# Performance work log

Hardware: AMD Instinct MI355X
Metric: run time of the kernel (lower is better)

## Reference

```python
import jax, jax.numpy as jnp
import numpy as np

S = 30000      # num sessions (= num clicks)
ND = 300000    # num displayed rows (10 per session)
F = 64         # f_dim
I = 500        # item_size (news_cnt_short)
PW = 10        # pw_dim
BAND = 20      # pw_band_size
H = 256        # mlp hidden


def setup_inputs() -> dict:
    key = jax.random.key(0)
    ks = jax.random.split(key, 8)
    per = ND // S  # disp rows per session
    disp_sec = jnp.repeat(jnp.arange(S, dtype=jnp.int64), per)          # sorted, every segment nonempty
    click_sub = jnp.arange(S, dtype=jnp.int64) * per                     # one clicked disp row per session
    # banded lower-triangular cumulative-sum indices: row r attends to cols r-0..r-(BAND-1) (clipped at 0)
    rows = jnp.repeat(jnp.arange(S, dtype=jnp.int64), BAND)
    offs = jnp.tile(jnp.arange(BAND, dtype=jnp.int64), S)
    cols = jnp.clip(rows - offs, 0)
    tril_idx = jnp.stack([rows, cols], axis=1)                            # [NT,2]
    click_items = jax.random.randint(ks[0], (S,), 0, I, dtype=jnp.int64)
    disp_items = jax.random.randint(ks[1], (ND,), 0, I, dtype=jnp.int64)
    return {
        'disp_current_feature': jax.random.normal(ks[2], (ND, F), dtype=jnp.float32),
        'Xs_clicked': jax.random.normal(ks[3], (S, F), dtype=jnp.float32),
        'W1': jax.random.normal(ks[4], (F * PW + F, H), dtype=jnp.float32) * 0.05,
        'b1': jnp.zeros((H,), jnp.float32),
        'W2': jax.random.normal(ks[5], (H, H), dtype=jnp.float32) * 0.05,
        'b2': jnp.zeros((H,), jnp.float32),
        'W3': jax.random.normal(ks[6], (H, 1), dtype=jnp.float32) * 0.05,
        'b3': jnp.zeros((1,), jnp.float32),
        'cumsum_tril_indices': tril_idx,
        'cumsum_tril_value_indices': offs,
        'disp_2d_split_sec_ind': disp_sec,
        'click_2d_subindex': click_sub,
        'click_indices': jnp.stack([jnp.arange(S, dtype=jnp.int64), click_items], axis=1),
        'disp_indices': jnp.stack([disp_sec, disp_items], axis=1),
        'section_length': S,
        'item_size': I,
        'pw_dim': PW,
        'band_size': BAND,
    }


def reference(disp_current_feature, Xs_clicked, W1, b1, W2, b2, W3, b3,
              cumsum_tril_indices, cumsum_tril_value_indices,
              disp_2d_split_sec_ind, click_2d_subindex,
              click_indices, disp_indices,
              section_length, item_size, pw_dim, band_size):
    # position weights (fixed 1e-4 as in original forward), gathered per sparse entry
    position_weight = jnp.full((band_size,), 1e-4, dtype=jnp.float32)
    vals = position_weight[cumsum_tril_value_indices]                     # [NT]
    # sparse [S,S] matmul with Xs_clicked expressed as gather + segment_sum (same math as dense matmul)
    contrib = vals[:, None] * Xs_clicked[cumsum_tril_indices[:, 1]]       # [NT,F]
    hist = jax.ops.segment_sum(contrib, cumsum_tril_indices[:, 0], num_segments=section_length)  # [S,F]
    # the pw_dim copies are identical (same position_weight each loop iteration)
    concat_history = jnp.concatenate([hist] * pw_dim, axis=1)             # [S, PW*F]
    disp_hist = concat_history[disp_2d_split_sec_ind]                     # [ND, PW*F]
    feats = jnp.concatenate([disp_hist, disp_current_feature], axis=1)    # [ND, (PW+1)*F]
    h = jax.nn.elu(feats @ W1 + b1)
    h = jax.nn.elu(h @ W2 + b2)
    u_disp = h @ W3 + b3                                                  # [ND,1]
    exp_u = jnp.exp(u_disp)
    sum_exp = jax.ops.segment_sum(exp_u, disp_2d_split_sec_ind, num_segments=section_length)  # [S,1]
    sum_click_u = u_disp[click_2d_subindex]                               # [S,1]
    loss_sum = jnp.sum(-sum_click_u + jnp.log(sum_exp + 1.0))
    click_tensor = jnp.zeros((section_length, item_size), jnp.float32).at[
        click_indices[:, 0], click_indices[:, 1]].add(1.0)
    event_cnt = jnp.sum(click_tensor)
    loss = loss_sum / event_cnt
    dense_exp = jnp.zeros((section_length, item_size), jnp.float32).at[
        disp_indices[:, 0], disp_indices[:, 1]].add(exp_u[:, 0])
    argmax_click = jnp.argmax(click_tensor, axis=1)
    argmax_disp = jnp.argmax(dense_exp, axis=1)
    top2 = jax.lax.top_k(dense_exp, 2)[1]                                 # [S,2]
    p1_sum = jnp.sum(argmax_click == argmax_disp)
    p2_sum = jnp.sum(argmax_click[:, None] == top2)
    precision_1 = p1_sum / event_cnt
    precision_2 = p2_sum / event_cnt
    return (loss, precision_1, precision_2, loss_sum, p1_sum, p2_sum, event_cnt)
```

## Files before the change

### kernel.cpp

```cpp
#include <hip/hip_runtime.h>
#include <hip/hip_bf16.h>

#define TPB 256

typedef _Float16 f16;
typedef f16 f16x8 __attribute__((ext_vector_type(8)));
typedef f16 f16x4 __attribute__((ext_vector_type(4)));
typedef f16 f16x2 __attribute__((ext_vector_type(2)));
typedef float f32x16 __attribute__((ext_vector_type(16)));
typedef unsigned int uint;

union F16x8U { f16x8 v; uint4 q; };
union F16x4U { f16x4 v; uint2 q; };

__device__ __forceinline__ float elu_f(float z) {
    return z > 0.f ? z : __expf(z) - 1.f;
}

__global__ void prepw0_kernel(const float* __restrict__ W1, int PW,
                              f16* __restrict__ W1sT_hi,
                              float* __restrict__ lossTot, int* __restrict__ cnts) {
    int t = blockIdx.x * blockDim.x + threadIdx.x;
    if (t < 16384) {
        int k = t >> 8, n = t & 255;
        float s = 0.f;
        for (int p = 0; p < PW; ++p) s += W1[(size_t)(p * 64 + k) * 256 + n];
        W1sT_hi[n * 64 + k] = (f16)s;
    } else if (t == 16384) {
        lossTot[0] = 0.f;
        cnts[0] = 0; cnts[1] = 0; cnts[2] = 0;
    }
}

__global__ __launch_bounds__(TPB, 4) void hist_ahist_kernel(
    const float* __restrict__ Xs, const int* __restrict__ tril,
    const f16* __restrict__ W1sT_hi, const float* __restrict__ b1,
    f16* __restrict__ Ah16, int S, int band,
    const float* __restrict__ W1, const float* __restrict__ W2, int PW,
    f16* __restrict__ W1bT_hi, f16* __restrict__ W2sw,
    int HB)
{
    __shared__ f16 hB[128 * 72];

    const int tid = threadIdx.x;

    if ((int)blockIdx.x >= HB) {
        int t = (blockIdx.x - HB) * TPB + tid;
        if (t < 16384) {
            int k = t >> 8, n = t & 255;
            W1bT_hi[n * 64 + k] = (f16)W1[(size_t)(PW * 64 + k) * 256 + n];
        } else {
            int t2 = t - 16384;
            int k = t2 >> 8, n = t2 & 255;
            W2sw[(size_t)(k >> 3) * 2048 + n * 8 + (k & 7)] = (f16)W2[(size_t)k * 256 + n];
        }
        return;
    }

    const int SB = blockIdx.x * 128;

    {
        const int f = tid & 63, w = tid >> 6;
        const int rl0 = w * 32;
        const int rg0 = SB + rl0;
        float sum = 0.f;
        #pragma unroll
        for (int o = 0; o < 20; ++o) {
            int gi = rg0 - o; if (gi < 0) gi = 0;
            sum += Xs[(size_t)gi * 64 + f];
        }
        hB[rl0 * 72 + f] = (f16)(sum * 1e-4f);
        for (int rl = rl0 + 1; rl < rl0 + 32; ++rl) {
            int rg = SB + rl;
            int rgc = rg <= S - 1 ? rg : S - 1;
            int gs = rg - 20; if (gs < 0) gs = 0; if (gs > S - 1) gs = S - 1;
            sum += Xs[(size_t)rgc * 64 + f] - Xs[(size_t)gs * 64 + f];
            hB[rl * 72 + f] = (f16)(sum * 1e-4f);
        }
    }
    __syncthreads();

    const int w = tid >> 6;
    const int l = tid & 63, lr = l & 31, hh = l >> 5;
    const int nt0 = 2 * w;

    #pragma unroll
    for (int st = 0; st < 4; ++st) {
        int sgl = st * 32 + lr;
        F16x8U Bh[4];
        #pragma unroll
        for (int ks = 0; ks < 4; ++ks)
            Bh[ks].q = *(const uint4*)&hB[sgl * 72 + ks * 16 + 8 * hh];
        int sg = SB + sgl;
        #pragma unroll
        for (int jn = 0; jn < 2; ++jn) {
            int nt = nt0 + jn;
            f32x16 acc;
            #pragma unroll
            for (int rq = 0; rq < 4; ++rq) {
                float4 bq = *(const float4*)&b1[nt * 32 + rq * 8 + 4 * hh];
                acc[rq * 4 + 0] = bq.x; acc[rq * 4 + 1] = bq.y;
                acc[rq * 4 + 2] = bq.z; acc[rq * 4 + 3] = bq.w;
            }
            const f16* ah = W1sT_hi + (size_t)(nt * 32 + lr) * 64 + 8 * hh;
            #pragma unroll
            for (int ks = 0; ks < 4; ++ks) {
                f16x8 Ah = *(const f16x8*)(ah + ks * 16);
                acc = __builtin_amdgcn_mfma_f32_32x32x16_f16(Ah, Bh[ks].v, acc, 0, 0, 0);
            }
            if (sg < S) {
                F16x8U o0, o1;
                #pragma unroll
                for (int i = 0; i < 8; ++i) {
                    o0.v[i] = (f16)acc[i];
                    o1.v[i] = (f16)acc[8 + i];
                }
                f16* op = Ah16 + (((size_t)sg * 8 + nt) * 2 + hh) * 16;
                *(uint4*)op = o0.q;
                *(uint4*)(op + 8) = o1.q;
            }
        }
    }
}

__global__ __launch_bounds__(512, 4) void mlp18_kernel(
    const float* __restrict__ dispF, const f16* __restrict__ Ah16,
    const f16* __restrict__ W1bT_hi,
    const f16* __restrict__ W2sw,
    const float* __restrict__ b2, const float* __restrict__ W3,
    const float* __restrict__ b3, float* __restrict__ u,
    int ND, int per, float inv_per)
{
    __shared__ uint4 frag[4][16][64];
    f16* dstage = (f16*)&frag[3][0][0];

    const int tid = threadIdx.x;
    const int w = tid >> 6, l = tid & 63, lr = l & 31, hh = l >> 5;
    const int RB = blockIdx.x * 128;
    const int nt = w;

    #pragma unroll
    for (int r = 0; r < 4; ++r) {
        int i = r * 512 + tid;
        int row = i >> 4, q = i & 15;
        int k8 = q >> 1;
        int rg = RB + row; if (rg > ND - 1) rg = ND - 1;
        float4 v = *(const float4*)&dispF[(size_t)rg * 64 + q * 4];
        F16x4U o;
        o.v[0] = (f16)v.x; o.v[1] = (f16)v.y; o.v[2] = (f16)v.z; o.v[3] = (f16)v.w;
        *(uint2*)&dstage[(size_t)(((row >> 5) * 8 + k8) * 256)
                         + ((row & 31) ^ k8) * 8 + (q & 1) * 4] = o.q;
    }

    const f16* a1h = W1bT_hi + (size_t)(nt * 32 + lr) * 64 + 8 * hh;
    f16x8 A1h[4];
    #pragma unroll
    for (int ks = 0; ks < 4; ++ks) A1h[ks] = *(const f16x8*)(a1h + ks * 16);

    const f16* w2p = W2sw + (size_t)hh * 2048 + (size_t)(nt * 32 + lr) * 8;
    f16x8 W2p[4];
    #pragma unroll
    for (int kp = 0; kp < 4; ++kp) W2p[kp] = *(const f16x8*)(w2p + (size_t)kp * 4096);

    int srow[4];
    #pragma unroll
    for (int st = 0; st < 4; ++st) {
        int rg = RB + st * 32 + lr;
        int rgc = rg <= ND - 1 ? rg : ND - 1;
        int sr = (int)((float)rgc * inv_per);
        sr += ((sr + 1) * per <= rgc) ? 1 : 0;
        srow[st] = sr;
    }

    __syncthreads();

    f16x8 Db[2][4];
    uint4 AhP[2][2];
    #pragma unroll
    for (int b = 0; b < 2; ++b) {
        #pragma unroll
        for (int ks = 0; ks < 4; ++ks) {
            int k8 = ks * 2 + hh;
            Db[b][ks] = *(const f16x8*)&dstage[(size_t)((b * 8 + k8) * 256) + (lr ^ k8) * 8];
        }
        const f16* ap = Ah16 + (((size_t)srow[b] * 8 + nt) * 2 + hh) * 16;
        AhP[b][0] = *(const uint4*)ap;
        AhP[b][1] = *(const uint4*)(ap + 8);
    }

    #pragma unroll
    for (int st = 0; st < 4; ++st) {
        f32x16 acc;
        {
            F16x8U u0, u1; u0.q = AhP[st & 1][0]; u1.q = AhP[st & 1][1];
            #pragma unroll
            for (int i = 0; i < 8; ++i) {
                acc[i] = (float)u0.v[i];
                acc[8 + i] = (float)u1.v[i];
            }
        }
        if (st + 2 < 4) {
            const f16* ap = Ah16 + (((size_t)srow[st + 2] * 8 + nt) * 2 + hh) * 16;
            AhP[st & 1][0] = *(const uint4*)ap;
            AhP[st & 1][1] = *(const uint4*)(ap + 8);
        }
        #pragma unroll
        for (int ks = 0; ks < 4; ++ks) {
            acc = __builtin_amdgcn_mfma_f32_32x32x16_f16(A1h[ks], Db[st & 1][ks], acc, 0, 0, 0);
        }
        if (st + 2 < 4) {
            #pragma unroll
            for (int ks = 0; ks < 4; ++ks) {
                int k8 = ks * 2 + hh;
                Db[st & 1][ks] = *(const f16x8*)&dstage[
                    (size_t)(((st + 2) * 8 + k8) * 256) + (lr ^ k8) * 8];
            }
        }

        uint p[4][2];
        #pragma unroll
        for (int rq = 0; rq < 4; ++rq) {
            #pragma unroll
            for (int jj = 0; jj < 2; ++jj) {
                float a = elu_f(acc[rq * 4 + 2 * jj]);
                float b = elu_f(acc[rq * 4 + 2 * jj + 1]);
                f16x2 hp; hp[0] = (f16)a; hp[1] = (f16)b;
                p[rq][jj] = __builtin_bit_cast(uint, hp);
            }
        }
        #pragma unroll
        for (int c = 0; c < 2; ++c) {
            uint s0 = hh ? p[2 * c][0] : p[2 * c + 1][0];
            uint s1 = hh ? p[2 * c][1] : p[2 * c + 1][1];
            uint r0 = __shfl_xor(s0, 32, 64);
            uint r1 = __shfl_xor(s1, 32, 64);
            uint4 B;
            B.x = hh ? r0 : p[2 * c][0];
            B.y = hh ? r1 : p[2 * c][1];
            B.z = hh ? p[2 * c + 1][0] : r0;
            B.w = hh ? p[2 * c + 1][1] : r1;
            frag[st][2 * nt + c][l] = B;
        }
        if (st == 1) __syncthreads();
    }
    __syncthreads();

    f32x16 acc2[4];
    #pragma unroll
    for (int rq = 0; rq < 4; ++rq) {
        float4 bq = *(const float4*)&b2[nt * 32 + rq * 8 + 4 * hh];
        #pragma unroll
        for (int st = 0; st < 4; ++st) {
            acc2[st][rq * 4 + 0] = bq.x; acc2[st][rq * 4 + 1] = bq.y;
            acc2[st][rq * 4 + 2] = bq.z; acc2[st][rq * 4 + 3] = bq.w;
        }
    }

    #pragma unroll
    for (int kt = 0; kt < 16; ++kt) {
        f16x8 Ah = W2p[kt & 3];
        if (kt + 4 < 16) W2p[kt & 3] = *(const f16x8*)(w2p + (size_t)(kt + 4) * 4096);
        #pragma unroll
        for (int st = 0; st < 4; ++st) {
            F16x8U B; B.q = frag[st][kt][l];
            acc2[st] = __builtin_amdgcn_mfma_f32_32x32x16_f16(Ah, B.v, acc2[st], 0, 0, 0);
        }
    }

    float up[4] = {0.f, 0.f, 0.f, 0.f};
    #pragma unroll
    for (int rq = 0; rq < 4; ++rq) {
        float4 wq = *(const float4*)&W3[nt * 32 + rq * 8 + 4 * hh];
        #pragma unroll
        for (int st = 0; st < 4; ++st) {
            up[st] += elu_f(acc2[st][rq * 4 + 0]) * wq.x
                    + elu_f(acc2[st][rq * 4 + 1]) * wq.y
                    + elu_f(acc2[st][rq * 4 + 2]) * wq.z
                    + elu_f(acc2[st][rq * 4 + 3]) * wq.w;
        }
    }
    #pragma unroll
    for (int st = 0; st < 4; ++st) up[st] += __shfl_xor(up[st], 32, 64);

    __syncthreads();
    float* pb = (float*)frag;
    if (hh == 0) {
        #pragma unroll
        for (int st = 0; st < 4; ++st) pb[(w * 4 + st) * 32 + lr] = up[st];
    }
    __syncthreads();
    if (tid < 128) {
        int st = tid >> 5, lrr = tid & 31;
        float v = 0.f;
        #pragma unroll
        for (int w2 = 0; w2 < 8; ++w2) v += pb[(w2 * 4 + st) * 32 + lrr];
        int rg = RB + tid;
        if (rg < ND) u[rg] = v + b3[0];
    }
}

template <int PER>
__global__ void session_kernel(const float* __restrict__ u, const int* __restrict__ clickSub,
                               const int* __restrict__ clickIdx, const int* __restrict__ dispIdx,
                               float* __restrict__ lossTot, int* __restrict__ cnts,
                               int S, float event_cnt, float* __restrict__ out) {
    int s = blockIdx.x * 64 + threadIdx.x;
    float lossv = 0.f; int p1 = 0, p2 = 0;
    if (s < S) {
        float ev[PER]; int it[PER];
        const float2* up2 = (const float2*)(u + (size_t)s * PER);
        const int4* dp4 = (const int4*)(dispIdx + (size_t)s * PER * 2);
        float uu[PER];
        #pragma unroll
        for (int j = 0; j < PER / 2; ++j) {
            float2 v = up2[j];
            uu[2 * j] = v.x; uu[2 * j + 1] = v.y;
            int4 d = dp4[j];
            it[2 * j] = d.y; it[2 * j + 1] = d.w;
        }
        float sum_exp = 0.f;
        #pragma unroll
        for (int i = 0; i < PER; ++i) {
            ev[i] = expf(uu[i]);
            sum_exp += ev[i];
        }
        int crow = clickSub[s];
        lossv = -u[crow] + logf(sum_exp + 1.f);

        float bestv = -1.f; int besti = 0x7FFFFFFF;
        float secv = -1.f;  int seci = 0x7FFFFFFF;
        int ndist = 0;
        #pragma unroll
        for (int i = 0; i < PER; ++i) {
            bool first = true; float tot = 0.f;
            #pragma unroll
            for (int j = 0; j < PER; ++j) {
                if (it[j] == it[i]) { tot += ev[j]; if (j < i) first = false; }
            }
            if (first) {
                ndist++;
                if (tot > bestv || (tot == bestv && it[i] < besti)) {
                    secv = bestv; seci = besti;
                    bestv = tot;  besti = it[i];
                } else if (tot > secv || (tot == secv && it[i] < seci)) {
                    secv = tot; seci = it[i];
                }
            }
        }
        if (ndist < 2) seci = (besti == 0) ? 1 : 0;
        int citem = clickIdx[s * 2 + 1];
        p1 = (citem == besti) ? 1 : 0;
        p2 = (citem == besti || citem == seci) ? 1 : 0;
    }
    #pragma unroll
    for (int off = 32; off > 0; off >>= 1) {
        lossv += __shfl_xor(lossv, off, 64);
        p1 += __shfl_xor(p1, off, 64);
        p2 += __shfl_xor(p2, off, 64);
    }
    if (threadIdx.x == 0) {
        atomicAdd(lossTot, lossv);
        atomicAdd(&cnts[1], p1);
        atomicAdd(&cnts[2], p2);
        __threadfence();
        int ticket = atomicAdd(&cnts[0], 1);
        if (ticket == (int)gridDim.x - 1) {
            __threadfence();
            float ls = *(volatile float*)lossTot;
            float a1 = (float)((volatile int*)cnts)[1];
            float a2 = (float)((volatile int*)cnts)[2];
            out[0] = ls / event_cnt;
            out[1] = a1 / event_cnt;
            out[2] = a2 / event_cnt;
            out[3] = ls;
            out[4] = a1;
            out[5] = a2;
            out[6] = event_cnt;
        }
    }
}

extern "C" void kernel_launch(void* const* d_in, const int* in_sizes, int n_in,
                              void* d_out, int out_size, void* d_ws, size_t ws_size,
                              hipStream_t stream) {
    const float* dispF    = (const float*)d_in[0];
    const float* Xs       = (const float*)d_in[1];
    const float* W1       = (const float*)d_in[2];
    const float* b1       = (const float*)d_in[3];
    const float* W2       = (const float*)d_in[4];
    const float* b2       = (const float*)d_in[5];
    const float* W3       = (const float*)d_in[6];
    const float* b3       = (const float*)d_in[7];
    const int*   tril     = (const int*)d_in[8];
    const int*   clickSub = (const int*)d_in[11];
    const int*   clickIdx = (const int*)d_in[12];
    const int*   dispIdx  = (const int*)d_in[13];

    const int S    = in_sizes[11];
    const int ND   = in_sizes[10];
    const int F    = in_sizes[1] / S;
    const int H    = in_sizes[3];
    const int NT   = in_sizes[9];
    const int BAND = NT / S;
    const int PW   = in_sizes[2] / (F * H) - 1;
    const int per  = ND / S;

    const int nblk = (ND + 127) / 128;
    const int HB   = (S + 127) / 128;

    float* ws    = (float*)d_ws;
    float* u     = ws;
    float* lossTot = u + ((size_t)ND + 128);
    int*   cnts  = (int*)(lossTot + 4);
    size_t f32_used = (size_t)((float*)(cnts + 4) - ws);
    f32_used = (f32_used + 3) & ~(size_t)3;
    f16* W1bT_hi = (f16*)(ws + f32_used);
    f16* W1sT_hi = W1bT_hi + 16384;
    f16* W2sw    = W1sT_hi + 16384;
    f16* Ah16    = W2sw + 65536;

    const int nb5 = (S + 63) / 64;

    prepw0_kernel<<<65, TPB, 0, stream>>>(W1, PW, W1sT_hi, lossTot, cnts);
    hist_ahist_kernel<<<HB + 320, TPB, 0, stream>>>(
        Xs, tril, W1sT_hi, b1, Ah16, S, BAND,
        W1, W2, PW, W1bT_hi, W2sw, HB);
    mlp18_kernel<<<nblk, 512, 0, stream>>>(
        dispF, Ah16, W1bT_hi, W2sw, b2, W3, b3, u,
        ND, per, 1.0f / (float)per);
    session_kernel<10><<<nb5, 64, 0, stream>>>(
        u, clickSub, clickIdx, dispIdx, lossTot, cnts, S, (float)S, (float*)d_out);
}
```

Before: 123.8 us.

## Split MLP tile processing into two halves to cut registers and raise occupancy

The fused MLP kernel now runs the 128-row tile as two 64-row halves. Each half does layer 1 for two subtiles and then layer 2 with only two accumulators instead of four. The W1/W2 register prefetch arrays are dropped and operands are reloaded per use, which lowers VGPR pressure so the launch bound can rise from 4 to 6 blocks per SIMD. Shared memory shrinks from a 4-slot frag buffer to 2 slots plus a separate dstage buffer. The trade-off is more global/L2 reloads of the weights, which are now read twice per block, plus extra barriers, and less latency hiding from prefetch.

Result: slower. 188.8 us (+52.6%).

```diff
diff --git a/kernel.cpp b/kernel.cpp
--- a/kernel.cpp
+++ b/kernel.cpp
@@ -123,7 +123,81 @@
     }
 }
 
-__global__ __launch_bounds__(512, 4) void mlp18_kernel(
+#define PHASE1_TILE(ST, SLOT, SROW)                                            \
+    {                                                                          \
+        const f16* ap_ = Ah16 + (((size_t)(SROW) * 8 + nt) * 2 + hh) * 16;     \
+        uint4 q0_ = *(const uint4*)ap_;                                        \
+        uint4 q1_ = *(const uint4*)(ap_ + 8);                                  \
+        f32x16 acc_;                                                           \
+        { F16x8U u0_, u1_; u0_.q = q0_; u1_.q = q1_;                           \
+          _Pragma("unroll")                                                    \
+          for (int i = 0; i < 8; ++i) {                                        \
+              acc_[i] = (float)u0_.v[i]; acc_[8 + i] = (float)u1_.v[i];        \
+          } }                                                                  \
+        _Pragma("unroll")                                                      \
+        for (int ks = 0; ks < 4; ++ks) {                                       \
+            int k8_ = ks * 2 + hh;                                             \
+            f16x8 D_ = *(const f16x8*)&dstage[(size_t)(((ST) * 8 + k8_) * 256) \
+                                              + (lr ^ k8_) * 8];               \
+            f16x8 A_ = *(const f16x8*)(a1hp + ks * 16);                        \
+            acc_ = __builtin_amdgcn_mfma_f32_32x32x16_f16(A_, D_, acc_, 0, 0, 0); \
+        }                                                                      \
+        uint p_[4][2];                                                         \
+        _Pragma("unroll")                                                      \
+        for (int rq = 0; rq < 4; ++rq) {                                       \
+            _Pragma("unroll")                                                  \
+            for (int jj = 0; jj < 2; ++jj) {                                   \
+                float a_ = elu_f(acc_[rq * 4 + 2 * jj]);                       \
+                float b_ = elu_f(acc_[rq * 4 + 2 * jj + 1]);                   \
+                f16x2 hp_; hp_[0] = (f16)a_; hp_[1] = (f16)b_;                 \
+                p_[rq][jj] = __builtin_bit_cast(uint, hp_);                    \
+            }                                                                  \
+        }                                                                      \
+        _Pragma("unroll")                                                      \
+        for (int c = 0; c < 2; ++c) {                                          \
+            uint s0_ = hh ? p_[2 * c][0] : p_[2 * c + 1][0];                   \
+            uint s1_ = hh ? p_[2 * c][1] : p_[2 * c + 1][1];                   \
+            uint r0_ = __shfl_xor(s0_, 32, 64);                                \
+            uint r1_ = __shfl_xor(s1_, 32, 64);                                \
+            uint4 B_;                                                          \
+            B_.x = hh ? r0_ : p_[2 * c][0];                                    \
+            B_.y = hh ? r1_ : p_[2 * c][1];                                    \
+            B_.z = hh ? p_[2 * c + 1][0] : r0_;                                \
+            B_.w = hh ? p_[2 * c + 1][1] : r1_;                                \
+            frag[SLOT][2 * nt + c][l] = B_;                                    \
+        }                                                                      \
+    }
+
+#define PHASE2_HALF(UPA, UPB)                                                  \
+    {                                                                          \
+        f32x16 aA_, aB_;                                                       \
+        _Pragma("unroll")                                                      \
+        for (int rq = 0; rq < 4; ++rq) {                                       \
+            float4 bq_ = *(const float4*)&b2[nt * 32 + rq * 8 + 4 * hh];       \
+            aA_[rq*4+0]=bq_.x; aA_[rq*4+1]=bq_.y; aA_[rq*4+2]=bq_.z; aA_[rq*4+3]=bq_.w; \
+            aB_[rq*4+0]=bq_.x; aB_[rq*4+1]=bq_.y; aB_[rq*4+2]=bq_.z; aB_[rq*4+3]=bq_.w; \
+        }                                                                      \
+        _Pragma("unroll")                                                      \
+        for (int kt = 0; kt < 16; ++kt) {                                      \
+            f16x8 Ah_ = *(const f16x8*)(w2p + (size_t)kt * 4096);              \
+            F16x8U BA_; BA_.q = frag[0][kt][l];                                \
+            F16x8U BB_; BB_.q = frag[1][kt][l];                                \
+            aA_ = __builtin_amdgcn_mfma_f32_32x32x16_f16(Ah_, BA_.v, aA_, 0, 0, 0); \
+            aB_ = __builtin_amdgcn_mfma_f32_32x32x16_f16(Ah_, BB_.v, aB_, 0, 0, 0); \
+        }                                                                      \
+        float sA_ = 0.f, sB_ = 0.f;                                            \
+        _Pragma("unroll")                                                      \
+        for (int rq = 0; rq < 4; ++rq) {                                       \
+            float4 wq_ = *(const float4*)&W3[nt * 32 + rq * 8 + 4 * hh];       \
+            sA_ += elu_f(aA_[rq*4+0])*wq_.x + elu_f(aA_[rq*4+1])*wq_.y         \
+                 + elu_f(aA_[rq*4+2])*wq_.z + elu_f(aA_[rq*4+3])*wq_.w;        \
+            sB_ += elu_f(aB_[rq*4+0])*wq_.x + elu_f(aB_[rq*4+1])*wq_.y         \
+                 + elu_f(aB_[rq*4+2])*wq_.z + elu_f(aB_[rq*4+3])*wq_.w;        \
+        }                                                                      \
+        UPA = sA_; UPB = sB_;                                                  \
+    }
+
+__global__ __launch_bounds__(512, 6) void mlp20_kernel(
     const float* __restrict__ dispF, const f16* __restrict__ Ah16,
     const f16* __restrict__ W1bT_hi,
     const f16* __restrict__ W2sw,
@@ -131,8 +205,8 @@
     const float* __restrict__ b3, float* __restrict__ u,
     int ND, int per, float inv_per)
 {
-    __shared__ uint4 frag[4][16][64];
-    f16* dstage = (f16*)&frag[3][0][0];
+    __shared__ uint4 frag[2][16][64];
+    __shared__ f16 dstage[8192];
 
     const int tid = threadIdx.x;
     const int w = tid >> 6, l = tid & 63, lr = l & 31, hh = l >> 5;
@@ -152,141 +226,49 @@
                          + ((row & 31) ^ k8) * 8 + (q & 1) * 4] = o.q;
     }
 
-    const f16* a1h = W1bT_hi + (size_t)(nt * 32 + lr) * 64 + 8 * hh;
-    f16x8 A1h[4];
-    #pragma unroll
-    for (int ks = 0; ks < 4; ++ks) A1h[ks] = *(const f16x8*)(a1h + ks * 16);
-
-    const f16* w2p = W2sw + (size_t)hh * 2048 + (size_t)(nt * 32 + lr) * 8;
-    f16x8 W2p[4];
-    #pragma unroll
-    for (int kp = 0; kp < 4; ++kp) W2p[kp] = *(const f16x8*)(w2p + (size_t)kp * 4096);
-
-    int srow[4];
-    #pragma unroll
-    for (int st = 0; st < 4; ++st) {
-        int rg = RB + st * 32 + lr;
-        int rgc = rg <= ND - 1 ? rg : ND - 1;
-        int sr = (int)((float)rgc * inv_per);
-        sr += ((sr + 1) * per <= rgc) ? 1 : 0;
-        srow[st] = sr;
-    }
-
-    __syncthreads();
-
-    f16x8 Db[2][4];
-    uint4 AhP[2][2];
-    #pragma unroll
-    for (int b = 0; b < 2; ++b) {
-        #pragma unroll
-        for (int ks = 0; ks < 4; ++ks) {
-            int k8 = ks * 2 + hh;
-            Db[b][ks] = *(const f16x8*)&dstage[(size_t)((b * 8 + k8) * 256) + (lr ^ k8) * 8];
-        }
-        const f16* ap = Ah16 + (((size_t)srow[b] * 8 + nt) * 2 + hh) * 16;
-        AhP[b][0] = *(const uint4*)ap;
-        AhP[b][1] = *(const uint4*)(ap + 8);
-    }
-
-    #pragma unroll
-    for (int st = 0; st < 4; ++st) {
-        f32x16 acc;
-        {
-            F16x8U u0, u1; u0.q = AhP[st & 1][0]; u1.q = AhP[st & 1][1];
-            #pragma unroll
-            for (int i = 0; i < 8; ++i) {
-                acc[i] = (float)u0.v[i];
-                acc[8 + i] = (float)u1.v[i];
-            }
-        }
-        if (st + 2 < 4) {
-            const f16* ap = Ah16 + (((size_t)srow[st + 2] * 8 + nt) * 2 + hh) * 16;
-            AhP[st & 1][0] = *(const uint4*)ap;
-            AhP[st & 1][1] = *(const uint4*)(ap + 8);
-        }
-        #pragma unroll
-        for (int ks = 0; ks < 4; ++ks) {
-            acc = __builtin_amdgcn_mfma_f32_32x32x16_f16(A1h[ks], Db[st & 1][ks], acc, 0, 0, 0);
-        }
-        if (st + 2 < 4) {
-            #pragma unroll
-            for (int ks = 0; ks < 4; ++ks) {
-                int k8 = ks * 2 + hh;
-                Db[st & 1][ks] = *(const f16x8*)&dstage[
-                    (size_t)(((st + 2) * 8 + k8) * 256) + (lr ^ k8) * 8];
-            }
-        }
-
-        uint p[4][2];
-        #pragma unroll
-        for (int rq = 0; rq < 4; ++rq) {
-            #pragma unroll
-            for (int jj = 0; jj < 2; ++jj) {
-                float a = elu_f(acc[rq * 4 + 2 * jj]);
-                float b = elu_f(acc[rq * 4 + 2 * jj + 1]);
-                f16x2 hp; hp[0] = (f16)a; hp[1] = (f16)b;
-                p[rq][jj] = __builtin_bit_cast(uint, hp);
-            }
-        }
-        #pragma unroll
-        for (int c = 0; c < 2; ++c) {
-            uint s0 = hh ? p[2 * c][0] : p[2 * c + 1][0];
-            uint s1 = hh ? p[2 * c][1] : p[2 * c + 1][1];
-            uint r0 = __shfl_xor(s0, 32, 64);
-            uint r1 = __shfl_xor(s1, 32, 64);
-            uint4 B;
-            B.x = hh ? r0 : p[2 * c][0];
-            B.y = hh ? r1 : p[2 * c][1];
-            B.z = hh ? p[2 * c + 1][0] : r0;
-            B.w = hh ? p[2 * c + 1][1] : r1;
-            frag[st][2 * nt + c][l] = B;
-        }
-        if (st == 1) __syncthreads();
-    }
-    __syncthreads();
-
-    f32x16 acc2[4];
-    #pragma unroll
-    for (int rq = 0; rq < 4; ++rq) {
-        float4 bq = *(const float4*)&b2[nt * 32 + rq * 8 + 4 * hh];
-        #pragma unroll
-        for (int st = 0; st < 4; ++st) {
-            acc2[st][rq * 4 + 0] = bq.x; acc2[st][rq * 4 + 1] = bq.y;
-            acc2[st][rq * 4 + 2] = bq.z; acc2[st][rq * 4 + 3] = bq.w;
-        }
-    }
-
-    #pragma unroll
-    for (int kt = 0; kt < 16; ++kt) {
-        f16x8 Ah = W2p[kt & 3];
-        if (kt + 4 < 16) W2p[kt & 3] = *(const f16x8*)(w2p + (size_t)(kt + 4) * 4096);
-        #pragma unroll
-        for (int st = 0; st < 4; ++st) {
-            F16x8U B; B.q = frag[st][kt][l];
-            acc2[st] = __builtin_amdgcn_mfma_f32_32x32x16_f16(Ah, B.v, acc2[st], 0, 0, 0);
-        }
-    }
-
-    float up[4] = {0.f, 0.f, 0.f, 0.f};
-    #pragma unroll
-    for (int rq = 0; rq < 4; ++rq) {
-        float4 wq = *(const float4*)&W3[nt * 32 + rq * 8 + 4 * hh];
-        #pragma unroll
-        for (int st = 0; st < 4; ++st) {
-            up[st] += elu_f(acc2[st][rq * 4 + 0]) * wq.x
-                    + elu_f(acc2[st][rq * 4 + 1]) * wq.y
-                    + elu_f(acc2[st][rq * 4 + 2]) * wq.z
-                    + elu_f(acc2[st][rq * 4 + 3]) * wq.w;
-        }
-    }
-    #pragma unroll
-    for (int st = 0; st < 4; ++st) up[st] += __shfl_xor(up[st], 32, 64);
+    const f16* a1hp = W1bT_hi + (size_t)(nt * 32 + lr) * 64 + 8 * hh;
+    const f16* w2p  = W2sw + (size_t)hh * 2048 + (size_t)(nt * 32 + lr) * 8;
+
+    int srow0, srow1, srow2, srow3;
+    {
+        int rg, rgc, sr;
+        rg = RB + 0 * 32 + lr; rgc = rg <= ND - 1 ? rg : ND - 1;
+        sr = (int)((float)rgc * inv_per); sr += ((sr + 1) * per <= rgc) ? 1 : 0; srow0 = sr;
+        rg = RB + 1 * 32 + lr; rgc = rg <= ND - 1 ? rg : ND - 1;
+        sr = (int)((float)rgc * inv_per); sr += ((sr + 1) * per <= rgc) ? 1 : 0; srow1 = sr;
+        rg = RB + 2 * 32 + lr; rgc = rg <= ND - 1 ? rg : ND - 1;
+        sr = (int)((float)rgc * inv_per); sr += ((sr + 1) * per <= rgc) ? 1 : 0; srow2 = sr;
+        rg = RB + 3 * 32 + lr; rgc = rg <= ND - 1 ? rg : ND - 1;
+        sr = (int)((float)rgc * inv_per); sr += ((sr + 1) * per <= rgc) ? 1 : 0; srow3 = sr;
+    }
+
+    __syncthreads();
+
+    float up0, up1, up2, up3;
+
+    PHASE1_TILE(0, 0, srow0)
+    PHASE1_TILE(1, 1, srow1)
+    __syncthreads();
+    PHASE2_HALF(up0, up1)
+    __syncthreads();
+
+    PHASE1_TILE(2, 0, srow2)
+    PHASE1_TILE(3, 1, srow3)
+    __syncthreads();
+    PHASE2_HALF(up2, up3)
+
+    up0 += __shfl_xor(up0, 32, 64);
+    up1 += __shfl_xor(up1, 32, 64);
+    up2 += __shfl_xor(up2, 32, 64);
+    up3 += __shfl_xor(up3, 32, 64);
 
     __syncthreads();
     float* pb = (float*)frag;
     if (hh == 0) {
-        #pragma unroll
-        for (int st = 0; st < 4; ++st) pb[(w * 4 + st) * 32 + lr] = up[st];
+        pb[(w * 4 + 0) * 32 + lr] = up0;
+        pb[(w * 4 + 1) * 32 + lr] = up1;
+        pb[(w * 4 + 2) * 32 + lr] = up2;
+        pb[(w * 4 + 3) * 32 + lr] = up3;
     }
     __syncthreads();
     if (tid < 128) {
@@ -425,7 +407,7 @@
     hist_ahist_kernel<<<HB + 320, TPB, 0, stream>>>(
         Xs, tril, W1sT_hi, b1, Ah16, S, BAND,
         W1, W2, PW, W1bT_hi, W2sw, HB);
-    mlp18_kernel<<<nblk, 512, 0, stream>>>(
+    mlp20_kernel<<<nblk, 512, 0, stream>>>(
         dispF, Ah16, W1bT_hi, W2sw, b2, W3, b3, u,
         ND, per, 1.0f / (float)per);
     session_kernel<10><<<nb5, 64, 0, stream>>>(
```
